# Optimization experiments

Hardware: AMD Instinct MI355X
Metric: run time of the kernel (lower is better)

Reference implementation:

```python
import jax, jax.numpy as jnp
import numpy as np

N_HEAD = 16
HEAD_DIM = 64
N_EMBD = N_HEAD * HEAD_DIM  # 1024


def setup_inputs() -> dict:
    key = jax.random.key(0)
    ks = jax.random.split(key, 5)
    B, S = 2, 2048
    x = jax.random.normal(ks[0], (B, S, N_EMBD), dtype=jnp.float32)
    qkv_w = jax.random.normal(ks[1], (N_EMBD, 3 * N_EMBD), dtype=jnp.float32) * 0.02
    qkv_b = jax.random.normal(ks[2], (3 * N_EMBD,), dtype=jnp.float32) * 0.02
    proj_w = jax.random.normal(ks[3], (N_EMBD, N_EMBD), dtype=jnp.float32) * 0.02
    proj_b = jax.random.normal(ks[4], (N_EMBD,), dtype=jnp.float32) * 0.02
    return {"x": x, "qkv_w": qkv_w, "qkv_b": qkv_b, "proj_w": proj_w, "proj_b": proj_b}


def reference(x, qkv_w, qkv_b, proj_w, proj_b):
    B, S, _ = x.shape
    qkv = x @ qkv_w + qkv_b  # [B,S,3E]
    q, k, v = jnp.split(qkv, 3, axis=-1)
    # [B,H,S,D]
    q = q.reshape(B, S, N_HEAD, HEAD_DIM).transpose(0, 2, 1, 3)
    k = k.reshape(B, S, N_HEAD, HEAD_DIM).transpose(0, 2, 1, 3)
    v = v.reshape(B, S, N_HEAD, HEAD_DIM).transpose(0, 2, 1, 3)
    scale = 1.0 / jnp.sqrt(jnp.float32(HEAD_DIM))
    scores = jnp.einsum('bhqd,bhkd->bhqk', q, k) * scale  # [B,H,S,S]
    causal = jnp.tril(jnp.ones((S, S), dtype=bool))
    scores = jnp.where(causal[None, None], scores, jnp.float32(-jnp.inf))
    attn = jax.nn.softmax(scores, axis=-1)  # dropout p=0 (eval)
    out = jnp.einsum('bhqk,bhkd->bhqd', attn, v)
    out = out.transpose(0, 2, 1, 3).reshape(B, S, N_EMBD)
    out = out @ proj_w + proj_b  # resid dropout p=0
    return out, k, v
```

## Files before the change

### kernel.cpp

```cpp
#include <hip/hip_runtime.h>
#include <hip/hip_bf16.h>


typedef __attribute__((ext_vector_type(4))) float f32x4;
typedef __attribute__((ext_vector_type(16))) float f32x16;
typedef __attribute__((ext_vector_type(8))) short s16x8;
typedef __attribute__((ext_vector_type(4))) short s16x4;

__device__ __forceinline__ short f2bf(float f) {
    union { float f; unsigned u; } x{f};
    unsigned r = x.u + 0x7fff + ((x.u >> 16) & 1);
    return (short)(r >> 16);
}

__device__ __forceinline__ void gload_lds16(const void* g, void* l) {
    __builtin_amdgcn_global_load_lds(
        (const __attribute__((address_space(1))) void*)g,
        (__attribute__((address_space(3))) void*)l, 16, 0, 0);
}

__global__ __launch_bounds__(256) void fused_prepass(const float* __restrict__ x,
                                                     short* __restrict__ x_bf,
                                                     const float* __restrict__ qkv_w,
                                                     short* __restrict__ wT1,
                                                     const float* __restrict__ proj_w,
                                                     short* __restrict__ wT2) {
    __shared__ float tile[32][33];
    const int bid = blockIdx.x, tid = threadIdx.x;
    if (bid < 2048) {
        int i = (bid * 256 + tid) * 8;
        f32x4 a = *(const f32x4*)&x[i];
        f32x4 b = *(const f32x4*)&x[i + 4];
        s16x8 o;
        #pragma unroll
        for (int j = 0; j < 4; ++j) o[j] = f2bf(a[j]);
        #pragma unroll
        for (int j = 0; j < 4; ++j) o[j + 4] = f2bf(b[j]);
        *(s16x8*)&x_bf[i] = o;
        return;
    }
    const float* in;
    short* out;
    int K = 1024, N, n0, k0;
    if (bid < 5120) {
        int blk = bid - 2048;
        in = qkv_w; out = wT1; N = 3072;
        n0 = (blk % 96) * 32; k0 = (blk / 96) * 32;
    } else {
        int blk = bid - 5120;
        in = proj_w; out = wT2; N = 1024;
        n0 = (blk & 31) * 32; k0 = (blk >> 5) * 32;
    }
    const int tx = tid & 31, ty = tid >> 5;
    #pragma unroll
    for (int r = 0; r < 4; ++r)
        tile[ty + r * 8][tx] = in[(long)(k0 + ty + r * 8) * N + n0 + tx];
    __syncthreads();
    #pragma unroll
    for (int r = 0; r < 4; ++r)
        out[(long)(n0 + ty + r * 8) * K + k0 + tx] = f2bf(tile[tx][ty + r * 8]);
}

__global__ __launch_bounds__(256) void gemm1_bf16(
    const short* __restrict__ A, const short* __restrict__ Bt,
    const float* __restrict__ bias, int M, int N, int K,
    short* __restrict__ qbf, short* __restrict__ kbf, short* __restrict__ vbfT,
    float* __restrict__ kout, float* __restrict__ vout) {
    __shared__ __align__(16) short As[128 * 64];
    __shared__ __align__(16) short Bs[96 * 64];
    const int tid = threadIdx.x;
    const int l = tid & 63, w = tid >> 6;
    const int lr = l >> 4, lc = l & 15;
    const int wm = w >> 1, wn = w & 1;
    const int bid = blockIdx.x;
    const int xcd = bid & 7, s = bid >> 3;
    const int bx = (xcd & 1) * 16 + (s & 15);
    const int by = (xcd >> 1) * 8 + (s >> 4);
    const int m0 = by * 128, n0 = bx * 96;

    f32x4 acc[4][3] = {};

    for (int kb = 0; kb < K; kb += 64) {
        __syncthreads();
        #pragma unroll
        for (int j = 0; j < 4; ++j) {
            const int c = tid + 256 * j;
            const int row = c >> 3;
            const int lseg = (c & 7) ^ (row & 7);
            gload_lds16(A + (long)(m0 + row) * K + kb + lseg * 8, As + c * 8);
            if (j < 3)
                gload_lds16(Bt + (long)(n0 + row) * K + kb + lseg * 8, Bs + c * 8);
        }
        __syncthreads();
        #pragma unroll
        for (int kh = 0; kh < 2; ++kh) {
            s16x8 af[4], bfr[3];
            #pragma unroll
            for (int mi = 0; mi < 4; ++mi) {
                const int row = wm * 64 + mi * 16 + lc;
                af[mi] = *(const s16x8*)&As[row * 64 + (((kh * 4 + lr) ^ (lc & 7)) * 8)];
            }
            #pragma unroll
            for (int ni = 0; ni < 3; ++ni) {
                const int row = wn * 48 + ni * 16 + lc;
                bfr[ni] = *(const s16x8*)&Bs[row * 64 + (((kh * 4 + lr) ^ (lc & 7)) * 8)];
            }
            #pragma unroll
            for (int mi = 0; mi < 4; ++mi)
                #pragma unroll
                for (int ni = 0; ni < 3; ++ni)
                    acc[mi][ni] = __builtin_amdgcn_mfma_f32_16x16x32_bf16(
                        af[mi], bfr[ni], acc[mi][ni], 0, 0, 0);
        }
    }

    #pragma unroll
    for (int mi = 0; mi < 4; ++mi) {
        #pragma unroll
        for (int ni = 0; ni < 3; ++ni) {
            int col = n0 + wn * 48 + ni * 16 + lc;
            float bv = bias[col];
            int sec = col >> 10, rem = col & 1023;
            int h = rem >> 6, d = rem & 63;
            int row0 = m0 + wm * 64 + mi * 16 + lr * 4;
            int b = row0 >> 11, s0 = row0 & 2047;
            long idxSD = ((long)((b << 4) + h) * 2048 + s0) * 64 + d;
            if (sec == 0) {
                #pragma unroll
                for (int i = 0; i < 4; ++i) {
                    float val = acc[mi][ni][i] + bv;
                    qbf[idxSD + (long)i * 64] = f2bf(val * 0.1803368801111244f);
                }
            } else if (sec == 1) {
                #pragma unroll
                for (int i = 0; i < 4; ++i) {
                    float val = acc[mi][ni][i] + bv;
                    kout[idxSD + (long)i * 64] = val;
                    kbf[idxSD + (long)i * 64] = f2bf(val);
                }
            } else {
                s16x4 pk;
                #pragma unroll
                for (int i = 0; i < 4; ++i) {
                    float val = acc[mi][ni][i] + bv;
                    vout[idxSD + (long)i * 64] = val;
                    pk[i] = f2bf(val);
                }
                *(s16x4*)&vbfT[((long)((b << 4) + h) * 64 + d) * 2048 + s0] = pk;
            }
        }
    }
}

__global__ __launch_bounds__(512) void gemm2_bf16(
    const short* __restrict__ A, const short* __restrict__ Bt,
    const float* __restrict__ bias, int M, int N, int K,
    float* __restrict__ outf) {
    __shared__ __align__(16) short As[2][128 * 64];
    __shared__ __align__(16) short Bs[2][128 * 64];
    const int tid = threadIdx.x;
    const int l = tid & 63, wv = tid >> 6;
    const int grp = wv >> 2, w = wv & 3;
    const int lr = l >> 4, lc = l & 15;
    const int wm = w >> 1, wn = w & 1;
    const int bid = blockIdx.x;
    const int xcd = bid & 7, s = bid >> 3;
    const int bx = (xcd & 1) * 4 + (s & 3), by = (xcd >> 1) * 8 + (s >> 2);
    const int m0 = by * 128, n0 = bx * 128;
    const int gtid = tid & 255;

    f32x4 acc[4][4] = {};

    for (int it = 0; it < 8; ++it) {
        const int kb = grp * 512 + it * 64;
        __syncthreads();
        #pragma unroll
        for (int j = 0; j < 4; ++j) {
            const int c = gtid + 256 * j;
            const int row = c >> 3;
            const int lseg = (c & 7) ^ (row & 7);
            gload_lds16(A + (long)(m0 + row) * K + kb + lseg * 8, &As[grp][c * 8]);
            gload_lds16(Bt + (long)(n0 + row) * K + kb + lseg * 8, &Bs[grp][c * 8]);
        }
        __syncthreads();
        #pragma unroll
        for (int kh = 0; kh < 2; ++kh) {
            s16x8 af[4], bfr[4];
            #pragma unroll
            for (int mi = 0; mi < 4; ++mi) {
                const int row = wm * 64 + mi * 16 + lc;
                af[mi] = *(const s16x8*)&As[grp][row * 64 + (((kh * 4 + lr) ^ (lc & 7)) * 8)];
            }
            #pragma unroll
            for (int ni = 0; ni < 4; ++ni) {
                const int row = wn * 64 + ni * 16 + lc;
                bfr[ni] = *(const s16x8*)&Bs[grp][row * 64 + (((kh * 4 + lr) ^ (lc & 7)) * 8)];
            }
            #pragma unroll
            for (int mi = 0; mi < 4; ++mi)
                #pragma unroll
                for (int ni = 0; ni < 4; ++ni)
                    acc[mi][ni] = __builtin_amdgcn_mfma_f32_16x16x32_bf16(
                        af[mi], bfr[ni], acc[mi][ni], 0, 0, 0);
        }
    }

    __syncthreads();
    float* reg = (w < 2) ? (float*)&As[w][0] : (float*)&Bs[w - 2][0];
    if (grp == 1) {
        #pragma unroll
        for (int mi = 0; mi < 4; ++mi)
            #pragma unroll
            for (int ni = 0; ni < 4; ++ni)
                #pragma unroll
                for (int i = 0; i < 4; ++i)
                    reg[(mi * 16 + lr * 4 + i) * 64 + ni * 16 + lc] = acc[mi][ni][i];
    }
    __syncthreads();
    if (grp == 1) return;
    #pragma unroll
    for (int mi = 0; mi < 4; ++mi)
        #pragma unroll
        for (int ni = 0; ni < 4; ++ni)
            #pragma unroll
            for (int i = 0; i < 4; ++i)
                acc[mi][ni][i] += reg[(mi * 16 + lr * 4 + i) * 64 + ni * 16 + lc];

    #pragma unroll
    for (int mi = 0; mi < 4; ++mi) {
        #pragma unroll
        for (int ni = 0; ni < 4; ++ni) {
            int col = n0 + wn * 64 + ni * 16 + lc;
            float bv = bias[col];
            #pragma unroll
            for (int i = 0; i < 4; ++i) {
                int row = m0 + wm * 64 + mi * 16 + lr * 4 + i;
                outf[(long)row * N + col] = acc[mi][ni][i] + bv;
            }
        }
    }
}

__global__ __launch_bounds__(512, 4) void attn_kernel(const short* __restrict__ qbf,
                                                      const short* __restrict__ kbf,
                                                      const short* __restrict__ vbfT,
                                                      short* __restrict__ obf) {
    const int bid = blockIdx.x;
    const int xcd = bid & 7, r = bid >> 3;
    const int head_local = r & 3, q16 = r >> 2;
    const int qt = (q16 < 8) ? (q16 + 8) : (15 - q16);
    const int bh = xcd * 4 + head_local;
    const int tid = threadIdx.x;
    const int wv = tid >> 6, l = tid & 63;
    const int strip = wv & 3, kh = wv >> 2;
    const int h = l >> 5;
    const int l8 = l & 7;
    const int q0 = qt * 128 + strip * 32;
    const int qlane = q0 + (l & 31);
    const long baseSD = (long)bh * 2048 * 64;
    const long baseDS = (long)bh * 64 * 2048;

    __shared__ __align__(16) short Ks[2][64 * 64];
    __shared__ __align__(16) short Vs[2][64 * 64];
    __shared__ __align__(16) float MG[4][64][36];

    const int sSub = l >> 3;
    const int sChunk = (l & 7) ^ sSub;
    auto stage = [&](int kt, int nb) {
        const int k0 = kt * 64;
        const int r0 = wv * 8 + sSub;
        gload_lds16(kbf + baseSD + (long)(k0 + r0) * 64 + sChunk * 8,
                    &Ks[nb][(wv * 8) * 64]);
        gload_lds16(vbfT + baseDS + (long)r0 * 2048 + k0 + sChunk * 8,
                    &Vs[nb][(wv * 8) * 64]);
    };

    s16x8 qf[4];
    #pragma unroll
    for (int dd = 0; dd < 4; ++dd)
        qf[dd] = *(const s16x8*)&qbf[baseSD + (long)qlane * 64 + dd * 16 + h * 8];

    f32x4 lacc = {};
    f32x16 O[2] = {};

    const int nkt = 2 * qt + 2;

    stage(0, 0);
    __syncthreads();
    int cur = 0;

    for (int kt = 0; kt < nkt; ++kt) {
        if (kt + 1 < nkt) stage(kt + 1, cur ^ 1);
        const int kbase = kt * 64 + kh * 32;

        if (kbase <= q0 + 31) {
            const short* Kb = Ks[cur];
            const short* Vb = Vs[cur];
            f32x16 z = {};
            #pragma unroll
            for (int dd = 0; dd < 4; ++dd) {
                s16x8 kf = *(const s16x8*)&Kb[(kh * 32 + (l & 31)) * 64 +
                                              (((2 * dd + h) ^ l8) * 8)];
                z = __builtin_amdgcn_mfma_f32_32x32x16_bf16(kf, qf[dd], z, 0, 0, 0);
            }
            if (kbase + 31 > q0) {
                #pragma unroll
                for (int rr = 0; rr < 16; ++rr) {
                    int kpos = kbase + (rr & 3) + 8 * (rr >> 2) + 4 * h;
                    if (kpos > qlane) z[rr] = -INFINITY;
                }
            }
            float p[16];
            #pragma unroll
            for (int rr = 0; rr < 16; ++rr) {
                p[rr] = __builtin_amdgcn_exp2f(z[rr]);
                lacc[rr & 3] += p[rr];
            }
            #pragma unroll
            for (int f = 0; f < 2; ++f) {
                union { __hip_bfloat162 b2[4]; s16x8 v; } pk;
                #pragma unroll
                for (int j = 0; j < 4; ++j)
                    pk.b2[j] = __float22bfloat162_rn(
                        make_float2(p[f * 8 + 2 * j], p[f * 8 + 2 * j + 1]));
                const int c0 = kh * 4 + f * 2;
                #pragma unroll
                for (int dt2 = 0; dt2 < 2; ++dt2) {
                    const short* vr = &Vb[(dt2 * 32 + (l & 31)) * 64];
                    s16x8 vf;
                    *(s16x4*)&vf = *(const s16x4*)&vr[(c0 ^ l8) * 8 + 4 * h];
                    *(((s16x4*)&vf) + 1) = *(const s16x4*)&vr[((c0 + 1) ^ l8) * 8 + 4 * h];
                    O[dt2] = __builtin_amdgcn_mfma_f32_32x32x16_bf16(vf, pk.v,
                                                                     O[dt2], 0, 0, 0);
                }
            }
        }
        __syncthreads();
        cur ^= 1;
    }

    float lsum = (lacc[0] + lacc[1]) + (lacc[2] + lacc[3]);
    if (kh == 1) {
        float* row = &MG[strip][l][0];
        #pragma unroll
        for (int dt2 = 0; dt2 < 2; ++dt2)
            #pragma unroll
            for (int rr = 0; rr < 16; ++rr)
                row[dt2 * 16 + rr] = O[dt2][rr];
        row[32] = lsum;
    }
    __syncthreads();
    if (kh == 0) {
        const float* row = &MG[strip][l][0];
        lsum += row[32];
        lsum += __shfl_xor(lsum, 32);
        const int b = bh >> 4, hd = bh & 15;
        float inv = 1.0f / lsum;
        #pragma unroll
        for (int dt2 = 0; dt2 < 2; ++dt2) {
            #pragma unroll
            for (int g = 0; g < 4; ++g) {
                s16x4 o;
                #pragma unroll
                for (int i = 0; i < 4; ++i)
                    o[i] = f2bf((O[dt2][g * 4 + i] + row[dt2 * 16 + g * 4 + i]) * inv);
                const int d = dt2 * 32 + 8 * g + 4 * h;
                *(s16x4*)&obf[(long)(b * 2048 + qlane) * 1024 + hd * 64 + d] = o;
            }
        }
    }
}


extern "C" void kernel_launch(void* const* d_in, const int* in_sizes, int n_in,
                              void* d_out, int out_size, void* d_ws, size_t ws_size,
                              hipStream_t stream) {
    const float* x = (const float*)d_in[0];
    const float* qkv_w = (const float*)d_in[1];
    const float* qkv_b = (const float*)d_in[2];
    const float* proj_w = (const float*)d_in[3];
    const float* proj_b = (const float*)d_in[4];

    float* out = (float*)d_out;
    float* kout = out + 4194304;
    float* vout = out + 8388608;

    short* x_bf = (short*)d_ws;
    short* wT1 = x_bf + 4194304;
    short* wT2 = wT1 + 3145728;
    short* q_bf = wT2 + 1048576;
    short* k_bf = q_bf + 4194304;
    short* vT_bf = k_bf + 4194304;
    short* o_bf = x_bf;

    fused_prepass<<<6144, 256, 0, stream>>>(x, x_bf, qkv_w, wT1, proj_w, wT2);

    gemm1_bf16<<<1024, 256, 0, stream>>>(x_bf, wT1, qkv_b, 4096, 3072, 1024,
                                         q_bf, k_bf, vT_bf, kout, vout);

    attn_kernel<<<512, 512, 0, stream>>>(q_bf, k_bf, vT_bf, o_bf);

    gemm2_bf16<<<256, 512, 0, stream>>>(o_bf, wT2, proj_b, 4096, 1024, 1024, out);
}
```

Before: 100.4 us.

## Reuse K/V LDS for attention merge buffer and raise occupancy target

Removes the separate 36KB merge buffer in the attention kernel and reuses the K/V staging LDS (32KB) for the cross-wave output merge, done in two half-passes with an XOR swizzle to avoid bank conflicts. Exp computation is moved inside the per-fragment loop to shorten register live ranges, and launch bounds request 6 blocks per CU instead of 4. The aim is lower LDS and register usage so more blocks fit per CU. The cost is two extra barriers in the epilogue and possible register spilling under the tighter bound.

```diff
diff --git a/kernel.cpp b/kernel.cpp
--- a/kernel.cpp
+++ b/kernel.cpp
@@ -241,7 +241,7 @@
     }
 }
 
-__global__ __launch_bounds__(512, 4) void attn_kernel(const short* __restrict__ qbf,
+__global__ __launch_bounds__(512, 6) void attn_kernel(const short* __restrict__ qbf,
                                                       const short* __restrict__ kbf,
                                                       const short* __restrict__ vbfT,
                                                       short* __restrict__ obf) {
@@ -262,7 +262,6 @@
 
     __shared__ __align__(16) short Ks[2][64 * 64];
     __shared__ __align__(16) short Vs[2][64 * 64];
-    __shared__ __align__(16) float MG[4][64][36];
 
     const int sSub = l >> 3;
     const int sChunk = (l & 7) ^ sSub;
@@ -310,19 +309,18 @@
                     if (kpos > qlane) z[rr] = -INFINITY;
                 }
             }
-            float p[16];
-            #pragma unroll
-            for (int rr = 0; rr < 16; ++rr) {
-                p[rr] = __builtin_amdgcn_exp2f(z[rr]);
-                lacc[rr & 3] += p[rr];
-            }
             #pragma unroll
             for (int f = 0; f < 2; ++f) {
+                float p[8];
+                #pragma unroll
+                for (int i = 0; i < 8; ++i) {
+                    p[i] = __builtin_amdgcn_exp2f(z[f * 8 + i]);
+                    lacc[i & 3] += p[i];
+                }
                 union { __hip_bfloat162 b2[4]; s16x8 v; } pk;
                 #pragma unroll
                 for (int j = 0; j < 4; ++j)
-                    pk.b2[j] = __float22bfloat162_rn(
-                        make_float2(p[f * 8 + 2 * j], p[f * 8 + 2 * j + 1]));
+                    pk.b2[j] = __float22bfloat162_rn(make_float2(p[2 * j], p[2 * j + 1]));
                 const int c0 = kh * 4 + f * 2;
                 #pragma unroll
                 for (int dt2 = 0; dt2 < 2; ++dt2) {
@@ -340,33 +338,46 @@
     }
 
     float lsum = (lacc[0] + lacc[1]) + (lacc[2] + lacc[3]);
+    float* OB = (float*)&Ks[0][0];
+    float* LB = (float*)&Vs[0][0];
+    const int slot = (strip * 64 + l) * 16;
+    const int b = bh >> 4, hd = bh & 15;
+    float inv = 0.f;
     if (kh == 1) {
-        float* row = &MG[strip][l][0];
-        #pragma unroll
-        for (int dt2 = 0; dt2 < 2; ++dt2)
-            #pragma unroll
-            for (int rr = 0; rr < 16; ++rr)
-                row[dt2 * 16 + rr] = O[dt2][rr];
-        row[32] = lsum;
+        #pragma unroll
+        for (int rr = 0; rr < 16; ++rr) OB[slot + (rr ^ (l & 15))] = O[0][rr];
+        LB[strip * 64 + l] = lsum;
     }
     __syncthreads();
     if (kh == 0) {
-        const float* row = &MG[strip][l][0];
-        lsum += row[32];
+        lsum += LB[strip * 64 + l];
         lsum += __shfl_xor(lsum, 32);
-        const int b = bh >> 4, hd = bh & 15;
-        float inv = 1.0f / lsum;
-        #pragma unroll
-        for (int dt2 = 0; dt2 < 2; ++dt2) {
-            #pragma unroll
-            for (int g = 0; g < 4; ++g) {
-                s16x4 o;
-                #pragma unroll
-                for (int i = 0; i < 4; ++i)
-                    o[i] = f2bf((O[dt2][g * 4 + i] + row[dt2 * 16 + g * 4 + i]) * inv);
-                const int d = dt2 * 32 + 8 * g + 4 * h;
-                *(s16x4*)&obf[(long)(b * 2048 + qlane) * 1024 + hd * 64 + d] = o;
-            }
+        inv = 1.0f / lsum;
+        #pragma unroll
+        for (int g = 0; g < 4; ++g) {
+            s16x4 o;
+            #pragma unroll
+            for (int i = 0; i < 4; ++i)
+                o[i] = f2bf((O[0][g * 4 + i] + OB[slot + ((g * 4 + i) ^ (l & 15))]) * inv);
+            const int d = 8 * g + 4 * h;
+            *(s16x4*)&obf[(long)(b * 2048 + qlane) * 1024 + hd * 64 + d] = o;
+        }
+    }
+    __syncthreads();
+    if (kh == 1) {
+        #pragma unroll
+        for (int rr = 0; rr < 16; ++rr) OB[slot + (rr ^ (l & 15))] = O[1][rr];
+    }
+    __syncthreads();
+    if (kh == 0) {
+        #pragma unroll
+        for (int g = 0; g < 4; ++g) {
+            s16x4 o;
+            #pragma unroll
+            for (int i = 0; i < 4; ++i)
+                o[i] = f2bf((O[1][g * 4 + i] + OB[slot + ((g * 4 + i) ^ (l & 15))]) * inv);
+            const int d = 32 + 8 * g + 4 * h;
+            *(s16x4*)&obf[(long)(b * 2048 + qlane) * 1024 + hd * 64 + d] = o;
         }
     }
 }
```

Result: slower. 154.2 us (+53.5%).
